# Kernel tuning notes

Measured on AMD Instinct MI355X. Metric: run time of the kernel, lower is better.

## Reference

```python
import jax, jax.numpy as jnp
import numpy as np

B, S, HID = 2, 2048, 2048
NH = 16
HD = HID // NH  # 128


def setup_inputs() -> dict:
    key = jax.random.key(0)
    ks = jax.random.split(key, 12)
    sc = 0.02
    return {
        "hidden_state": jax.random.normal(ks[0], (B, S, HID), jnp.float32),
        "attention_mask": jax.random.uniform(ks[1], (B, 1, S, S), jnp.float32),
        "Wq": jax.random.normal(ks[2], (HID, HID), jnp.float32) * sc,
        "bq": jnp.zeros((HID,), jnp.float32),
        "Wk": jax.random.normal(ks[3], (HD, HID), jnp.float32) * sc,
        "bk": jnp.zeros((HD,), jnp.float32),
        "Wv": jax.random.normal(ks[4], (HD, HID), jnp.float32) * sc,
        "bv": jnp.zeros((HD,), jnp.float32),
        "Wo": jax.random.normal(ks[5], (HID, HID), jnp.float32) * sc,
        "bo": jnp.zeros((HID,), jnp.float32),
    }


def reference(hidden_state, attention_mask, Wq, bq, Wk, bk, Wv, bv, Wo, bo):
    b = hidden_state.shape[0]
    # projections (nn.Linear: x @ W.T + b)
    q = hidden_state @ Wq.T + bq                      # [B,S,HID]
    k = hidden_state @ Wk.T + bk                      # [B,S,HD] (single shared head)
    v = hidden_state @ Wv.T + bv                      # [B,S,HD]
    # split heads: q -> [B,NH,S,HD]
    q = q.reshape(b, -1, NH, HD).transpose(0, 2, 1, 3)
    scale = jnp.sqrt(jnp.asarray(HD, q.dtype))
    scores = jnp.einsum('bhsd,btd->bhst', q, k) / scale  # [B,NH,S,S]
    # faithful to source: mask scaled by -1e-09 (as written)
    scores = scores + attention_mask * (-1e-09)
    probs = jax.nn.softmax(scores, axis=-1)
    out = jnp.einsum('bhst,btd->bhsd', probs, v)          # [B,NH,S,HD]
    # faithful to source: transpose(-1,-2) then flat view to [B,S,HID]
    out = out.transpose(0, 1, 3, 2).reshape(b, -1, HD * NH)
    return out @ Wo.T + bo
```

## Files before the change

kernel.cpp:

```cpp
#include <hip/hip_runtime.h>
#include <hip/hip_bf16.h>

#define BATCH 2
#define SEQ 2048
#define HIDDIM 2048
#define NHEADS 16
#define HDIM 128
#define QKVN 2304

typedef __attribute__((ext_vector_type(8))) short bf16x8;
typedef __attribute__((ext_vector_type(4))) short short4v;
typedef __attribute__((ext_vector_type(4))) float f32x4;
typedef __attribute__((ext_vector_type(16))) float f32x16;
typedef __attribute__((ext_vector_type(4))) unsigned u32x4;

__device__ __forceinline__ short f2bf(float f) {
  unsigned u = __builtin_bit_cast(unsigned, f);
  unsigned r = (u + 0x7fffu + ((u >> 16) & 1u)) >> 16;
  return (short)r;
}

__device__ __forceinline__ unsigned cvtpk_bf16(float a, float b) {
  unsigned r;
  asm("v_cvt_pk_bf16_f32 %0, %1, %2" : "=v"(r) : "v"(a), "v"(b));
  return r;
}

#define PLSWAP(a, b) asm("v_permlane32_swap_b32 %0, %1" : "+v"(a), "+v"(b))

__device__ __forceinline__ void gl_lds16(const void* g, void* l) {
  __builtin_amdgcn_global_load_lds(
      (const __attribute__((address_space(1))) void*)g,
      (__attribute__((address_space(3))) void*)l, 16, 0, 0);
}

__global__ void cvt_kernel(const float* __restrict__ in, short* __restrict__ out, int n) {
  int i = (blockIdx.x * blockDim.x + threadIdx.x) * 4;
  if (i >= n) return;
  float4 v = *(const float4*)(in + i);
  short4v o;
  o[0] = f2bf(v.x); o[1] = f2bf(v.y); o[2] = f2bf(v.z); o[3] = f2bf(v.w);
  *(short4v*)(out + i) = o;
}

__global__ void bias_concat(const float* __restrict__ bq, const float* __restrict__ bk,
                            const float* __restrict__ bv, float* __restrict__ out) {
  int i = blockIdx.x * 256 + threadIdx.x;
  if (i >= QKVN) return;
  float v;
  if (i < HIDDIM) v = bq[i];
  else if (i < HIDDIM + HDIM) v = bk[i - HIDDIM];
  else v = bv[i - HIDDIM - HDIM];
  out[i] = v;
}

template <int MODE>
__global__ __launch_bounds__(256, 2)
void gemm_bt(const short* __restrict__ A, const short* __restrict__ W,
             const float* __restrict__ bias, void* __restrict__ Cv, void* __restrict__ Cv2,
             int M, int N, int K, long sA, long sC)
{
  __shared__ short As[128 * 64];
  __shared__ short Ws[128 * 64];
  const int tid = threadIdx.x;
  const int lane = tid & 63;
  const int w = tid >> 6;
  const int wr = w >> 1, wc = w & 1;
  const int tm = blockIdx.y * 128, tn = blockIdx.x * 128;
  const short* Ap = A + (size_t)blockIdx.z * sA;

  const int rA = lane & 15;
  const int r7 = rA & 7;
  const int srow = lane >> 3;
  const int scg  = (lane & 7) ^ srow;

  f32x4 acc[4][4] = {};

  for (int k0 = 0; k0 < K; k0 += 64) {
    __syncthreads();
#pragma unroll
    for (int i = 0; i < 4; ++i) {
      int ch = w * 4 + i;
      gl_lds16(Ap + (size_t)(tm + ch * 8 + srow) * K + k0 + scg * 8, As + ch * 512);
      gl_lds16(W  + (size_t)(tn + ch * 8 + srow) * K + k0 + scg * 8, Ws + ch * 512);
    }
    __syncthreads();
#pragma unroll
    for (int kk = 0; kk < 64; kk += 32) {
      const int cg = (kk >> 3) + (lane >> 4);
      const int co = ((cg ^ r7) << 3);
      bf16x8 af[4];
#pragma unroll
      for (int mi = 0; mi < 4; ++mi)
        af[mi] = *(const bf16x8*)(As + ((wr * 64 + mi * 16 + rA) << 6) + co);
#pragma unroll
      for (int ni = 0; ni < 4; ++ni) {
        bf16x8 wf = *(const bf16x8*)(Ws + ((wc * 64 + ni * 16 + rA) << 6) + co);
#pragma unroll
        for (int mi = 0; mi < 4; ++mi)
          acc[mi][ni] = __builtin_amdgcn_mfma_f32_16x16x32_bf16(af[mi], wf, acc[mi][ni], 0, 0, 0);
      }
    }
  }

  const int cr = (lane >> 4) * 4;
  const int cc = lane & 15;
#pragma unroll
  for (int ni = 0; ni < 4; ++ni) {
    int col = tn + wc * 64 + ni * 16 + cc;
    float bv = bias[col];
#pragma unroll
    for (int mi = 0; mi < 4; ++mi) {
#pragma unroll
      for (int r = 0; r < 4; ++r) {
        int row = tm + wr * 64 + mi * 16 + cr + r;
        float v = acc[mi][ni][r] + bv;
        if constexpr (MODE == 0) {
          ((float*)Cv)[(size_t)blockIdx.z * sC + (size_t)row * N + col] = v;
        } else {
          if (col < HIDDIM + HDIM)
            ((short*)Cv)[(size_t)row * QKVN + col] = f2bf(v);
          else
            ((short*)Cv2)[(size_t)(col - HIDDIM - HDIM) * (BATCH * SEQ) + row] = f2bf(v);
        }
      }
    }
  }
}

__device__ __forceinline__ void stage_kv(const short* __restrict__ Kp,
                                         const short* __restrict__ Vt,
                                         short* buf, int b, int c, int tid) {
  const int lane = tid & 63;
  const int w = tid >> 6;
  const int rin = lane >> 4;
  const int gp = lane & 15;
#pragma unroll
  for (int i = 0; i < 4; ++i) {
    int ch = w * 4 + i;
    int row = ch * 4 + rin;
    int gl = gp ^ (row & 15);
    gl_lds16(Kp + (size_t)(b * SEQ + c * 128 + row) * QKVN + gl * 8, buf + ch * 512);
    gl_lds16(Vt + (size_t)row * (BATCH * SEQ) + b * SEQ + c * 128 + gl * 8,
             buf + 16384 + ch * 512);
  }
}

__global__ __launch_bounds__(512, 2)
void attn_kernel(const short* __restrict__ QKV, const short* __restrict__ Vt,
                 short* __restrict__ OT)
{
  __shared__ short smem[2][32768];
  const int tid = threadIdx.x;
  const int l31 = tid & 31;
  const int hi2 = (tid >> 5) & 1;
  const int w = tid >> 6;
  const int b = blockIdx.z, h = blockIdx.y, qt = blockIdx.x;
  const float C2 = 0.12752600954427384f;
  const short* Kp = QKV + HIDDIM;

  bf16x8 qf[8];
  {
    const short* Qp = QKV + (size_t)(b * SEQ + qt * 256 + w * 32 + l31) * QKVN + h * HDIM;
#pragma unroll
    for (int kk = 0; kk < 8; ++kk)
      qf[kk] = *(const bf16x8*)(Qp + kk * 16 + hi2 * 8);
  }

  f32x16 o[4] = {};
  float m = -1e30f, l = 0.f;

  stage_kv(Kp, Vt, smem[0], b, 0, tid);
  __syncthreads();

  for (int c = 0; c < 16; ++c) {
    const short* Ks = smem[c & 1];
    const short* Vs = smem[c & 1] + 16384;
    if (c < 15) stage_kv(Kp, Vt, smem[(c + 1) & 1], b, c + 1, tid);

    f32x16 s[4] = {};
#pragma unroll
    for (int n = 0; n < 4; ++n) {
      const int row = n * 32 + l31;
      const int rx = row & 15;
#pragma unroll
      for (int kk = 0; kk < 8; ++kk) {
        bf16x8 kf = *(const bf16x8*)(Ks + row * 128 + (((kk * 2 + hi2) ^ rx) << 3));
        s[n] = __builtin_amdgcn_mfma_f32_32x32x16_bf16(kf, qf[kk], s[n], 0, 0, 0);
      }
    }

    float mx = s[0][0];
#pragma unroll
    for (int n = 0; n < 4; ++n)
#pragma unroll
      for (int r = 0; r < 16; ++r) mx = fmaxf(mx, s[n][r]);
    mx = fmaxf(mx, __shfl_xor(mx, 32));
    mx *= C2;
    if (!__all(mx <= m + 8.f)) {
      float mn = fmaxf(m, mx);
      float cf = exp2f(m - mn);
      m = mn; l *= cf;
#pragma unroll
      for (int nd = 0; nd < 4; ++nd)
#pragma unroll
        for (int r = 0; r < 16; ++r) o[nd][r] *= cf;
    }

    u32x4 pw[4][2];
    float rs = 0.f;
#pragma unroll
    for (int n = 0; n < 4; ++n) {
      float p[16];
#pragma unroll
      for (int r = 0; r < 16; ++r) {
        p[r] = exp2f(__builtin_fmaf(s[n][r], C2, -m));
        rs += p[r];
      }
      unsigned w0 = cvtpk_bf16(p[0], p[1]),  w1 = cvtpk_bf16(p[2], p[3]);
      unsigned w2 = cvtpk_bf16(p[4], p[5]),  w3 = cvtpk_bf16(p[6], p[7]);
      unsigned w4 = cvtpk_bf16(p[8], p[9]),  w5 = cvtpk_bf16(p[10], p[11]);
      unsigned w6 = cvtpk_bf16(p[12], p[13]), w7 = cvtpk_bf16(p[14], p[15]);
      PLSWAP(w0, w2); PLSWAP(w1, w3);
      PLSWAP(w4, w6); PLSWAP(w5, w7);
      pw[n][0] = (u32x4){w0, w1, w2, w3};
      pw[n][1] = (u32x4){w4, w5, w6, w7};
    }
    rs += __shfl_xor(rs, 32);
    l += rs;

#pragma unroll
    for (int nd = 0; nd < 4; ++nd) {
      const int row = nd * 32 + l31;
      const int rx = row & 15;
#pragma unroll
      for (int n = 0; n < 4; ++n) {
#pragma unroll
        for (int t = 0; t < 2; ++t) {
          const int kvs = n * 2 + t;
          bf16x8 vf = *(const bf16x8*)(Vs + row * 128 + (((kvs * 2 + hi2) ^ rx) << 3));
          bf16x8 pa = __builtin_bit_cast(bf16x8, pw[n][t]);
          o[nd] = __builtin_amdgcn_mfma_f32_32x32x16_bf16(vf, pa, o[nd], 0, 0, 0);
        }
      }
    }
    __syncthreads();
  }

  const float inv = 1.f / l;
  short* dst = OT + (size_t)b * (SEQ * HIDDIM) + (size_t)(h * HDIM) * SEQ
             + qt * 256 + w * 32 + l31;
#pragma unroll
  for (int nd = 0; nd < 4; ++nd) {
#pragma unroll
    for (int r = 0; r < 16; ++r) {
      int d = nd * 32 + (r & 3) + 8 * (r >> 2) + 4 * hi2;
      dst[(size_t)d * SEQ] = f2bf(o[nd][r] * inv);
    }
  }
}

extern "C" void kernel_launch(void* const* d_in, const int* in_sizes, int n_in,
                              void* d_out, int out_size, void* d_ws, size_t ws_size,
                              hipStream_t stream)
{
  const float* hidden = (const float*)d_in[0];
  const float* Wq = (const float*)d_in[2];
  const float* bq = (const float*)d_in[3];
  const float* Wk = (const float*)d_in[4];
  const float* bk = (const float*)d_in[5];
  const float* Wv = (const float*)d_in[6];
  const float* bv = (const float*)d_in[7];
  const float* Wo = (const float*)d_in[8];
  const float* bo = (const float*)d_in[9];
  float* out = (float*)d_out;

  short* ws      = (short*)d_ws;
  short* QKV     = ws;
  short* Wo_bf   = ws;
  short* Vt_bf   = ws + 9437184;
  short* h_bf    = Vt_bf + 524288;
  short* OT      = h_bf;
  short* Wqkv_bf = h_bf + 8388608;
  float* bqkv    = (float*)(Wqkv_bf + 4718592);

  cvt_kernel<<<8192, 256, 0, stream>>>(hidden, h_bf, 8388608);
  cvt_kernel<<<4096, 256, 0, stream>>>(Wq, Wqkv_bf, 4194304);
  cvt_kernel<<<256,  256, 0, stream>>>(Wk, Wqkv_bf + 4194304, 262144);
  cvt_kernel<<<256,  256, 0, stream>>>(Wv, Wqkv_bf + 4456448, 262144);
  bias_concat<<<9, 256, 0, stream>>>(bq, bk, bv, bqkv);

  gemm_bt<3><<<dim3(18, 32, 1), 256, 0, stream>>>(h_bf, Wqkv_bf, bqkv, QKV, Vt_bf,
                                                  4096, QKVN, 2048, 0, 0);
  attn_kernel<<<dim3(8, 16, 2), 512, 0, stream>>>(QKV, Vt_bf, OT);
  cvt_kernel<<<4096, 256, 0, stream>>>(Wo, Wo_bf, 4194304);
  gemm_bt<0><<<dim3(16, 16, 2), 256, 0, stream>>>(OT, Wo_bf, bo, out, nullptr,
                                                  2048, 2048, 2048, 4194304, 4194304);
}
```

Before: 205.5 us.

## Merge conversion launches into one prep kernel and tune attention inner loop

The four fp32-to-bf16 conversion launches and the bias concatenation are folded into a single prep kernel, so fewer small kernels have to be launched. In the attention kernel, K/V staging pointers are computed once and then advanced each step instead of recomputing addresses per tile. The MFMA sections are wrapped in s_setprio to raise wave priority, and the row-max reduction uses a tree of three-input max operations. The combined prep kernel adds branching per block, and the priority hints may or may not help the wave scheduler.

```diff
diff --git a/kernel.cpp b/kernel.cpp
--- a/kernel.cpp
+++ b/kernel.cpp
@@ -32,6 +32,52 @@
   __builtin_amdgcn_global_load_lds(
       (const __attribute__((address_space(1))) void*)g,
       (__attribute__((address_space(3))) void*)l, 16, 0, 0);
+}
+
+__device__ __forceinline__ float max3f(float a, float b, float c) {
+  return fmaxf(fmaxf(a, b), c);
+}
+__device__ __forceinline__ float vmax16(const f32x16& v) {
+  float a = max3f(v[0], v[1], v[2]);
+  float b = max3f(v[3], v[4], v[5]);
+  float c = max3f(v[6], v[7], v[8]);
+  float d = max3f(v[9], v[10], v[11]);
+  float e = max3f(v[12], v[13], v[14]);
+  return fmaxf(max3f(a, b, c), max3f(d, e, v[15]));
+}
+
+__global__ void prep_kernel(const float* __restrict__ h, const float* __restrict__ Wq,
+                            const float* __restrict__ Wk, const float* __restrict__ Wv,
+                            const float* __restrict__ bq, const float* __restrict__ bk,
+                            const float* __restrict__ bv,
+                            short* __restrict__ h_bf, short* __restrict__ Wqkv_bf,
+                            float* __restrict__ bqkv)
+{
+  int bid = blockIdx.x;
+  const float* src;
+  short* dst;
+  int n;
+  if (bid < 8192)        { src = h;  dst = h_bf;                n = 8388608; }
+  else if (bid < 12288)  { src = Wq; dst = Wqkv_bf;             n = 4194304; bid -= 8192; }
+  else if (bid < 12544)  { src = Wk; dst = Wqkv_bf + 4194304;   n = 262144;  bid -= 12288; }
+  else if (bid < 12800)  { src = Wv; dst = Wqkv_bf + 4456448;   n = 262144;  bid -= 12544; }
+  else {
+    int i = (bid - 12800) * 256 + threadIdx.x;
+    if (i < QKVN) {
+      float v;
+      if (i < HIDDIM) v = bq[i];
+      else if (i < HIDDIM + HDIM) v = bk[i - HIDDIM];
+      else v = bv[i - HIDDIM - HDIM];
+      bqkv[i] = v;
+    }
+    return;
+  }
+  int i = (bid * 256 + threadIdx.x) * 4;
+  if (i >= n) return;
+  float4 v = *(const float4*)(src + i);
+  short4v o;
+  o[0] = f2bf(v.x); o[1] = f2bf(v.y); o[2] = f2bf(v.z); o[3] = f2bf(v.w);
+  *(short4v*)(dst + i) = o;
 }
 
 __global__ void cvt_kernel(const float* __restrict__ in, short* __restrict__ out, int n) {
@@ -41,17 +87,6 @@
   short4v o;
   o[0] = f2bf(v.x); o[1] = f2bf(v.y); o[2] = f2bf(v.z); o[3] = f2bf(v.w);
   *(short4v*)(out + i) = o;
-}
-
-__global__ void bias_concat(const float* __restrict__ bq, const float* __restrict__ bk,
-                            const float* __restrict__ bv, float* __restrict__ out) {
-  int i = blockIdx.x * 256 + threadIdx.x;
-  if (i >= QKVN) return;
-  float v;
-  if (i < HIDDIM) v = bq[i];
-  else if (i < HIDDIM + HDIM) v = bk[i - HIDDIM];
-  else v = bv[i - HIDDIM - HDIM];
-  out[i] = v;
 }
 
 template <int MODE>
@@ -128,24 +163,6 @@
   }
 }
 
-__device__ __forceinline__ void stage_kv(const short* __restrict__ Kp,
-                                         const short* __restrict__ Vt,
-                                         short* buf, int b, int c, int tid) {
-  const int lane = tid & 63;
-  const int w = tid >> 6;
-  const int rin = lane >> 4;
-  const int gp = lane & 15;
-#pragma unroll
-  for (int i = 0; i < 4; ++i) {
-    int ch = w * 4 + i;
-    int row = ch * 4 + rin;
-    int gl = gp ^ (row & 15);
-    gl_lds16(Kp + (size_t)(b * SEQ + c * 128 + row) * QKVN + gl * 8, buf + ch * 512);
-    gl_lds16(Vt + (size_t)row * (BATCH * SEQ) + b * SEQ + c * 128 + gl * 8,
-             buf + 16384 + ch * 512);
-  }
-}
-
 __global__ __launch_bounds__(512, 2)
 void attn_kernel(const short* __restrict__ QKV, const short* __restrict__ Vt,
                  short* __restrict__ OT)
@@ -159,6 +176,21 @@
   const float C2 = 0.12752600954427384f;
   const short* Kp = QKV + HIDDIM;
 
+  const short* kptr[4];
+  const short* vptr[4];
+  {
+    const int rin = (tid & 63) >> 4;
+    const int gp = tid & 15;
+#pragma unroll
+    for (int i = 0; i < 4; ++i) {
+      int ch = w * 4 + i;
+      int row = ch * 4 + rin;
+      int gl = gp ^ (row & 15);
+      kptr[i] = Kp + (size_t)(b * SEQ + row) * QKVN + gl * 8;
+      vptr[i] = Vt + (size_t)row * (BATCH * SEQ) + b * SEQ + gl * 8;
+    }
+  }
+
   bf16x8 qf[8];
   {
     const short* Qp = QKV + (size_t)(b * SEQ + qt * 256 + w * 32 + l31) * QKVN + h * HDIM;
@@ -170,15 +202,33 @@
   f32x16 o[4] = {};
   float m = -1e30f, l = 0.f;
 
-  stage_kv(Kp, Vt, smem[0], b, 0, tid);
+#pragma unroll
+  for (int i = 0; i < 4; ++i) {
+    int ch = w * 4 + i;
+    gl_lds16(kptr[i], (short*)smem[0] + ch * 512);
+    gl_lds16(vptr[i], (short*)smem[0] + 16384 + ch * 512);
+    kptr[i] += 128 * QKVN;
+    vptr[i] += 128;
+  }
   __syncthreads();
 
   for (int c = 0; c < 16; ++c) {
     const short* Ks = smem[c & 1];
     const short* Vs = smem[c & 1] + 16384;
-    if (c < 15) stage_kv(Kp, Vt, smem[(c + 1) & 1], b, c + 1, tid);
+    if (c < 15) {
+      short* nb = smem[(c + 1) & 1];
+#pragma unroll
+      for (int i = 0; i < 4; ++i) {
+        int ch = w * 4 + i;
+        gl_lds16(kptr[i], nb + ch * 512);
+        gl_lds16(vptr[i], nb + 16384 + ch * 512);
+        kptr[i] += 128 * QKVN;
+        vptr[i] += 128;
+      }
+    }
 
     f32x16 s[4] = {};
+    __builtin_amdgcn_s_setprio(1);
 #pragma unroll
     for (int n = 0; n < 4; ++n) {
       const int row = n * 32 + l31;
@@ -189,12 +239,10 @@
         s[n] = __builtin_amdgcn_mfma_f32_32x32x16_bf16(kf, qf[kk], s[n], 0, 0, 0);
       }
     }
-
-    float mx = s[0][0];
-#pragma unroll
-    for (int n = 0; n < 4; ++n)
-#pragma unroll
-      for (int r = 0; r < 16; ++r) mx = fmaxf(mx, s[n][r]);
+    __builtin_amdgcn_s_setprio(0);
+
+    float mx = fmaxf(fmaxf(vmax16(s[0]), vmax16(s[1])),
+                     fmaxf(vmax16(s[2]), vmax16(s[3])));
     mx = fmaxf(mx, __shfl_xor(mx, 32));
     mx *= C2;
     if (!__all(mx <= m + 8.f)) {
@@ -229,6 +277,7 @@
     rs += __shfl_xor(rs, 32);
     l += rs;
 
+    __builtin_amdgcn_s_setprio(1);
 #pragma unroll
     for (int nd = 0; nd < 4; ++nd) {
       const int row = nd * 32 + l31;
@@ -244,6 +293,7 @@
         }
       }
     }
+    __builtin_amdgcn_s_setprio(0);
     __syncthreads();
   }
 
@@ -284,11 +334,8 @@
   short* Wqkv_bf = h_bf + 8388608;
   float* bqkv    = (float*)(Wqkv_bf + 4718592);
 
-  cvt_kernel<<<8192, 256, 0, stream>>>(hidden, h_bf, 8388608);
-  cvt_kernel<<<4096, 256, 0, stream>>>(Wq, Wqkv_bf, 4194304);
-  cvt_kernel<<<256,  256, 0, stream>>>(Wk, Wqkv_bf + 4194304, 262144);
-  cvt_kernel<<<256,  256, 0, stream>>>(Wv, Wqkv_bf + 4456448, 262144);
-  bias_concat<<<9, 256, 0, stream>>>(bq, bk, bv, bqkv);
+  prep_kernel<<<12809, 256, 0, stream>>>(hidden, Wq, Wk, Wv, bq, bk, bv,
+                                         h_bf, Wqkv_bf, bqkv);
 
   gemm_bt<3><<<dim3(18, 32, 1), 256, 0, stream>>>(h_bf, Wqkv_bf, bqkv, QKV, Vt_bf,
                                                   4096, QKVN, 2048, 0, 0);
```

Measured after the change: 197.3 us. -4.0%, faster.
